# Kernel tuning notes

Measured on AMD Instinct MI355X. Metric: run time of the kernel, lower is better.

The kernel has to match this reference:

```python
import jax, jax.numpy as jnp
import numpy as np


def setup_inputs() -> dict:
    key = jax.random.key(0)
    kx, ky = jax.random.split(key)
    N, P1, P2, D = 4, 8192, 8192, 3
    x = jax.random.normal(kx, (N, P1, D), dtype=jnp.float32)
    y = jax.random.normal(ky, (N, P2, D), dtype=jnp.float32)
    return {"x": x, "y": y}


def reference(x, y):
    # ChamferDistance.forward with norm=2 (Euclidean cdist).
    N, P1, D = x.shape
    P2 = y.shape[1]
    x_sq = jnp.sum(x * x, axis=-1)              # [N, P1]
    y_sq = jnp.sum(y * y, axis=-1)              # [N, P2]
    xy = jnp.einsum("npd,nqd->npq", x, y)       # [N, P1, P2]
    sq = x_sq[:, :, None] + y_sq[:, None, :] - 2.0 * xy
    dists = jnp.sqrt(jnp.maximum(sq, 0.0))      # [N, P1, P2], == torch.cdist p=2
    cham_x = jnp.min(dists, axis=-1).sum(axis=1) / P1   # [N]
    cham_y = jnp.min(dists, axis=-2).sum(axis=1) / P2   # [N]
    return cham_x + cham_y
```

## Files before the change

kernel.cpp:

```cpp
#include <hip/hip_runtime.h>


typedef float v2f  __attribute__((ext_vector_type(2)));
typedef float v16f __attribute__((ext_vector_type(16)));

constexpr int BLK   = 256;
constexpr int Q     = 8;
constexpr int CHUNK = 128;
constexpr int NCH   = 64;

__global__ void preprocess_kernel(const float* __restrict__ X,
                                  const float* __restrict__ Y,
                                  float* __restrict__ pX, float* __restrict__ pY,
                                  unsigned int* __restrict__ wmin,
                                  float* __restrict__ out,
                                  int P1, int P2, int N)
{
    const int t  = blockIdx.x * blockDim.x + threadIdx.x;
    const int nx = N * P1;
    const int total = nx + N * P2;
    if (t < total) {
        const float* src = (t < nx) ? X : Y;
        float*       dst = (t < nx) ? pX : pY;
        const int    idx = (t < nx) ? t : t - nx;
        const float* p = src + 3L * idx;
        float x = p[0], y = p[1], z = p[2];
        float c = x * x + y * y + z * z;
        float* d = dst + (long)(idx >> 1) * 8;
        const int o = idx & 1;
        d[0 + o] = x; d[2 + o] = y; d[4 + o] = z; d[6 + o] = c;
        wmin[t] = 0xFFFFFFFFu;
    }
    if (t < N) out[t] = 0.f;
}

__global__ __launch_bounds__(BLK) void chamfer_min_kernel(
    const float* __restrict__ X, const float* __restrict__ Y,
    const float* __restrict__ pX, const float* __restrict__ pY,
    unsigned int* __restrict__ wmin, int P1, int P2, int N)
{
    const int n   = blockIdx.y;
    const int dz  = blockIdx.z;
    const int dir = dz / NCH;
    const int ch  = dz - dir * NCH;
    const float* A  = dir ? Y : X;
    const float* PB = dir ? pX : pY;
    const int Pa = dir ? P2 : P1;
    const int Pb = dir ? P1 : P2;

    const int stride = Pa / Q;
    const int ti = blockIdx.x * BLK + threadIdx.x;
    v2f nx[Q], ny[Q], nz[Q];
    float qsq[Q], m[Q];
    const float* An = A + (long)n * Pa * 3;
    #pragma unroll
    for (int q = 0; q < Q; ++q) {
        const float* p = An + 3L * (ti + q * stride);
        float ax = p[0], ay = p[1], az = p[2];
        nx[q].x = -2.f * ax; nx[q].y = nx[q].x;
        ny[q].x = -2.f * ay; ny[q].y = ny[q].x;
        nz[q].x = -2.f * az; nz[q].y = nz[q].x;
        qsq[q] = ax * ax + ay * ay + az * az;
        m[q] = 1e30f;
    }

    const float* pb = PB + ((long)n * (Pb >> 1) + (long)ch * (CHUNK >> 1)) * 8;

    auto compute4 = [&](const v16f& b) {
        v2f bx0; bx0.x = b[0];  bx0.y = b[1];
        v2f by0; by0.x = b[2];  by0.y = b[3];
        v2f bz0; bz0.x = b[4];  bz0.y = b[5];
        v2f cv0; cv0.x = b[6];  cv0.y = b[7];
        v2f bx1; bx1.x = b[8];  bx1.y = b[9];
        v2f by1; by1.x = b[10]; by1.y = b[11];
        v2f bz1; bz1.x = b[12]; bz1.y = b[13];
        v2f cv1; cv1.x = b[14]; cv1.y = b[15];
        #pragma unroll
        for (int q = 0; q < Q; ++q) {
            v2f t0, t1;
            asm("v_pk_fma_f32 %0, %2, %3, %4\n\t"
                "v_pk_fma_f32 %1, %2, %5, %6\n\t"
                "v_pk_fma_f32 %0, %7, %8, %0\n\t"
                "v_pk_fma_f32 %1, %7, %9, %1\n\t"
                "v_pk_fma_f32 %0, %10, %11, %0\n\t"
                "v_pk_fma_f32 %1, %10, %12, %1"
                : "=&v"(t0), "=&v"(t1)
                : "v"(nz[q]), "s"(bz0), "v"(cv0), "s"(bz1), "v"(cv1),
                  "v"(ny[q]), "s"(by0), "s"(by1),
                  "v"(nx[q]), "s"(bx0), "s"(bx1));
            float t0x = t0.x, t0y = t0.y, t1x = t1.x, t1y = t1.y;
            asm("v_min3_f32 %0, %1, %2, %0" : "+v"(m[q]) : "v"(t0x), "v"(t0y));
            asm("v_min3_f32 %0, %1, %2, %0" : "+v"(m[q]) : "v"(t1x), "v"(t1y));
        }
    };

    constexpr int NG = CHUNK / 4;
    v16f b0, b1;
    asm volatile("s_load_dwordx16 %0, %1, 0x0" : "=s"(b0) : "s"(pb));
    #pragma unroll 1
    for (int g = 0; g < NG; g += 2) {
        asm volatile("s_waitcnt lgkmcnt(0)" : "+s"(b0));
        if (g + 1 < NG)
            asm volatile("s_load_dwordx16 %0, %1, 0x0"
                         : "=s"(b1) : "s"(pb + (long)(g + 1) * 16));
        compute4(b0);
        asm volatile("s_waitcnt lgkmcnt(0)" : "+s"(b1));
        if (g + 2 < NG)
            asm volatile("s_load_dwordx16 %0, %1, 0x0"
                         : "=s"(b0) : "s"(pb + (long)(g + 2) * 16));
        compute4(b1);
    }

    unsigned int* wbase = wmin + (dir ? (long)N * P1 : 0) + (long)n * Pa;
    #pragma unroll
    for (int q = 0; q < Q; ++q) {
        float msq = fmaxf(m[q] + qsq[q], 0.0f);
        atomicMin(&wbase[ti + q * stride], __float_as_uint(msq));
    }
}

__global__ __launch_bounds__(BLK) void chamfer_reduce_kernel(
    const unsigned int* __restrict__ wmin, float* __restrict__ out,
    int P1, int P2, int N)
{
    __shared__ float wsum[BLK / 64];
    const int dir = blockIdx.z;
    const int n   = blockIdx.y;
    const int Pa  = dir ? P2 : P1;
    const unsigned int* base = wmin + (dir ? (long)N * P1 : 0) + (long)n * Pa;

    float s = 0.f;
    for (int i = blockIdx.x * BLK + threadIdx.x; i < Pa; i += gridDim.x * BLK)
        s += sqrtf(__uint_as_float(base[i]));

    for (int off = 32; off > 0; off >>= 1)
        s += __shfl_down(s, off);
    const int lane = threadIdx.x & 63, wid = threadIdx.x >> 6;
    if (lane == 0) wsum[wid] = s;
    __syncthreads();
    if (threadIdx.x == 0) {
        float t = 0.f;
        #pragma unroll
        for (int w = 0; w < BLK / 64; ++w) t += wsum[w];
        atomicAdd(&out[n], t / (float)Pa);
    }
}

extern "C" void kernel_launch(void* const* d_in, const int* in_sizes, int n_in,
                              void* d_out, int out_size, void* d_ws, size_t ws_size,
                              hipStream_t stream)
{
    const float* x = (const float*)d_in[0];
    const float* y = (const float*)d_in[1];
    float* out = (float*)d_out;

    const int N  = out_size;
    const int P1 = in_sizes[0] / (N * 3);
    const int P2 = in_sizes[1] / (N * 3);

    float* pX = (float*)d_ws;
    float* pY = pX + (long)N * P1 * 4;
    unsigned int* wmin = (unsigned int*)(pY + (long)N * P2 * 4);

    const int total = N * (P1 + P2);
    preprocess_kernel<<<(total + BLK - 1) / BLK, BLK, 0, stream>>>(
        x, y, pX, pY, wmin, out, P1, P2, N);

    const int gx = (max(P1, P2) / Q) / BLK;
    chamfer_min_kernel<<<dim3(gx, N, 2 * NCH), BLK, 0, stream>>>(
        x, y, pX, pY, wmin, P1, P2, N);

    chamfer_reduce_kernel<<<dim3(8, N, 2), BLK, 0, stream>>>(wmin, out, P1, P2, N);
}
```

Before: 52.53 us.

## Compute pairwise distance Gram terms with split-bf16 MFMA instead of packed FMA

Replaces the scalar/packed-FP32 distance loop with a matrix-core formulation. Each point's coordinates and squared norm are split into hi/lo bf16 pieces in preprocessing and packed into 16-element A/B vectors, so one 32x32x16 bf16 MFMA computes -2x·y + ||y||^2 with near-fp32 accuracy. Each wave keeps four 32-query B fragments resident, streams A fragments over a quarter of the targets, and folds the outputs with min3. The trade-off is a larger preprocessing workspace and reduced precision from the three-term bf16 split. The grid also assumes P1 == P2.

```diff
diff --git a/kernel.cpp b/kernel.cpp
--- a/kernel.cpp
+++ b/kernel.cpp
@@ -1,122 +1,140 @@
 #include <hip/hip_runtime.h>
 
 
-typedef float v2f  __attribute__((ext_vector_type(2)));
-typedef float v16f __attribute__((ext_vector_type(16)));
+typedef unsigned short u16;
+typedef short bf16x8 __attribute__((ext_vector_type(8)));
+typedef float f32x16 __attribute__((ext_vector_type(16)));
 
-constexpr int BLK   = 256;
-constexpr int Q     = 8;
-constexpr int CHUNK = 128;
-constexpr int NCH   = 64;
+constexpr int BLK = 256;
+constexpr int TC  = 4;
+
+__device__ __forceinline__ u16 f2bf(float f) {
+    unsigned u = __float_as_uint(f);
+    return (u16)((u + 0x7FFFu + ((u >> 16) & 1u)) >> 16);
+}
+__device__ __forceinline__ float bf2f(u16 h) {
+    return __uint_as_float((unsigned)h << 16);
+}
 
 __global__ void preprocess_kernel(const float* __restrict__ X,
                                   const float* __restrict__ Y,
-                                  float* __restrict__ pX, float* __restrict__ pY,
+                                  u16* __restrict__ AX, u16* __restrict__ BX,
+                                  u16* __restrict__ AY, u16* __restrict__ BY,
+                                  float* __restrict__ QSQ,
                                   unsigned int* __restrict__ wmin,
                                   float* __restrict__ out,
                                   int P1, int P2, int N)
 {
-    const int t  = blockIdx.x * blockDim.x + threadIdx.x;
+    const int t = blockIdx.x * blockDim.x + threadIdx.x;
     const int nx = N * P1;
     const int total = nx + N * P2;
     if (t < total) {
-        const float* src = (t < nx) ? X : Y;
-        float*       dst = (t < nx) ? pX : pY;
-        const int    idx = (t < nx) ? t : t - nx;
-        const float* p = src + 3L * idx;
-        float x = p[0], y = p[1], z = p[2];
-        float c = x * x + y * y + z * z;
-        float* d = dst + (long)(idx >> 1) * 8;
-        const int o = idx & 1;
-        d[0 + o] = x; d[2 + o] = y; d[4 + o] = z; d[6 + o] = c;
+        const bool isX = t < nx;
+        const int idx = isX ? t : t - nx;
+        const float* p = (isX ? X : Y) + 3L * idx;
+        float c[3] = {p[0], p[1], p[2]};
+        float tsq = fmaf(c[0], c[0], fmaf(c[1], c[1], c[2] * c[2]));
+        u16 uh[3], ul[3], qh[3], ql[3];
+        #pragma unroll
+        for (int i = 0; i < 3; ++i) {
+            float u = -2.f * c[i];
+            uh[i] = f2bf(u);    ul[i] = f2bf(u - bf2f(uh[i]));
+            qh[i] = f2bf(c[i]); ql[i] = f2bf(c[i] - bf2f(qh[i]));
+        }
+        u16 s1 = f2bf(tsq);
+        float r = tsq - bf2f(s1);
+        u16 s2 = f2bf(r);
+        u16 s3 = f2bf(r - bf2f(s2));
+        const u16 ONE = 0x3F80;
+        alignas(16) u16 av[16] = {uh[0],uh[1],uh[2], uh[0],uh[1],uh[2],
+                                  ul[0],ul[1],ul[2], ul[0],ul[1],ul[2],
+                                  s1, s2, s3, 0};
+        alignas(16) u16 bv[16] = {qh[0],qh[1],qh[2], ql[0],ql[1],ql[2],
+                                  qh[0],qh[1],qh[2], ql[0],ql[1],ql[2],
+                                  ONE, ONE, ONE, 0};
+        u16* ad = (isX ? AX : AY) + (size_t)idx * 16;
+        u16* bd = (isX ? BX : BY) + (size_t)idx * 16;
+        ((uint4*)ad)[0] = ((const uint4*)av)[0];
+        ((uint4*)ad)[1] = ((const uint4*)av)[1];
+        ((uint4*)bd)[0] = ((const uint4*)bv)[0];
+        ((uint4*)bd)[1] = ((const uint4*)bv)[1];
+        QSQ[t]  = tsq;
         wmin[t] = 0xFFFFFFFFu;
     }
     if (t < N) out[t] = 0.f;
 }
 
-__global__ __launch_bounds__(BLK) void chamfer_min_kernel(
-    const float* __restrict__ X, const float* __restrict__ Y,
-    const float* __restrict__ pX, const float* __restrict__ pY,
-    unsigned int* __restrict__ wmin, int P1, int P2, int N)
+__global__ __launch_bounds__(BLK) void chamfer_mfma_kernel(
+    const u16* __restrict__ AX, const u16* __restrict__ BX,
+    const u16* __restrict__ AY, const u16* __restrict__ BY,
+    const float* __restrict__ QSQ, unsigned int* __restrict__ wmin,
+    int P1, int P2, int N)
 {
-    const int n   = blockIdx.y;
-    const int dz  = blockIdx.z;
-    const int dir = dz / NCH;
-    const int ch  = dz - dir * NCH;
-    const float* A  = dir ? Y : X;
-    const float* PB = dir ? pX : pY;
-    const int Pa = dir ? P2 : P1;
-    const int Pb = dir ? P1 : P2;
+    const int n    = blockIdx.y;
+    const int dir  = blockIdx.z >> 2;
+    const int chk  = blockIdx.z & 3;
+    const int wave = threadIdx.x >> 6;
+    const int lane = threadIdx.x & 63;
+    const int col  = lane & 31;
+    const int half = lane >> 5;
 
-    const int stride = Pa / Q;
-    const int ti = blockIdx.x * BLK + threadIdx.x;
-    v2f nx[Q], ny[Q], nz[Q];
-    float qsq[Q], m[Q];
-    const float* An = A + (long)n * Pa * 3;
+    const int Pq = dir ? P2 : P1;
+    const int Pt = dir ? P1 : P2;
+    const u16* Bq = (dir ? BY : BX) + (size_t)n * Pq * 16;
+    const u16* At = (dir ? AX : AY) + (size_t)n * Pt * 16;
+    const float*  qs = QSQ  + (dir ? (size_t)N * P1 : 0) + (size_t)n * Pq;
+    unsigned int* wb = wmin + (dir ? (size_t)N * P1 : 0) + (size_t)n * Pq;
+
+    const int qg = blockIdx.x * (BLK / 64) + wave;
+    const int q0 = qg * 128 + col;
+    const bf16x8 b0 = *(const bf16x8*)(Bq + (size_t)(q0      ) * 16 + half * 8);
+    const bf16x8 b1 = *(const bf16x8*)(Bq + (size_t)(q0 +  32) * 16 + half * 8);
+    const bf16x8 b2 = *(const bf16x8*)(Bq + (size_t)(q0 +  64) * 16 + half * 8);
+    const bf16x8 b3 = *(const bf16x8*)(Bq + (size_t)(q0 +  96) * 16 + half * 8);
+    const float qs0 = qs[q0], qs1 = qs[q0 + 32], qs2 = qs[q0 + 64], qs3 = qs[q0 + 96];
+    float m0 = 1e30f, m1 = 1e30f, m2 = 1e30f, m3 = 1e30f;
+
+    f32x16 zc;
     #pragma unroll
-    for (int q = 0; q < Q; ++q) {
-        const float* p = An + 3L * (ti + q * stride);
-        float ax = p[0], ay = p[1], az = p[2];
-        nx[q].x = -2.f * ax; nx[q].y = nx[q].x;
-        ny[q].x = -2.f * ay; ny[q].y = ny[q].x;
-        nz[q].x = -2.f * az; nz[q].y = nz[q].x;
-        qsq[q] = ax * ax + ay * ay + az * az;
-        m[q] = 1e30f;
-    }
+    for (int i = 0; i < 16; ++i) zc[i] = 0.f;
 
-    const float* pb = PB + ((long)n * (Pb >> 1) + (long)ch * (CHUNK >> 1)) * 8;
+    #define MFMA(A, B) __builtin_amdgcn_mfma_f32_32x32x16_bf16((A), (B), zc, 0, 0, 0)
 
-    auto compute4 = [&](const v16f& b) {
-        v2f bx0; bx0.x = b[0];  bx0.y = b[1];
-        v2f by0; by0.x = b[2];  by0.y = b[3];
-        v2f bz0; bz0.x = b[4];  bz0.y = b[5];
-        v2f cv0; cv0.x = b[6];  cv0.y = b[7];
-        v2f bx1; bx1.x = b[8];  bx1.y = b[9];
-        v2f by1; by1.x = b[10]; by1.y = b[11];
-        v2f bz1; bz1.x = b[12]; bz1.y = b[13];
-        v2f cv1; cv1.x = b[14]; cv1.y = b[15];
+    auto fold = [&](const f32x16& d, float& mm) {
         #pragma unroll
-        for (int q = 0; q < Q; ++q) {
-            v2f t0, t1;
-            asm("v_pk_fma_f32 %0, %2, %3, %4\n\t"
-                "v_pk_fma_f32 %1, %2, %5, %6\n\t"
-                "v_pk_fma_f32 %0, %7, %8, %0\n\t"
-                "v_pk_fma_f32 %1, %7, %9, %1\n\t"
-                "v_pk_fma_f32 %0, %10, %11, %0\n\t"
-                "v_pk_fma_f32 %1, %10, %12, %1"
-                : "=&v"(t0), "=&v"(t1)
-                : "v"(nz[q]), "s"(bz0), "v"(cv0), "s"(bz1), "v"(cv1),
-                  "v"(ny[q]), "s"(by0), "s"(by1),
-                  "v"(nx[q]), "s"(bx0), "s"(bx1));
-            float t0x = t0.x, t0y = t0.y, t1x = t1.x, t1y = t1.y;
-            asm("v_min3_f32 %0, %1, %2, %0" : "+v"(m[q]) : "v"(t0x), "v"(t0y));
-            asm("v_min3_f32 %0, %1, %2, %0" : "+v"(m[q]) : "v"(t1x), "v"(t1y));
+        for (int i = 0; i < 16; i += 2) {
+            float x0 = d[i], x1 = d[i + 1];
+            asm("v_min3_f32 %0, %1, %2, %0" : "+v"(mm) : "v"(x0), "v"(x1));
         }
     };
 
-    constexpr int NG = CHUNK / 4;
-    v16f b0, b1;
-    asm volatile("s_load_dwordx16 %0, %1, 0x0" : "=s"(b0) : "s"(pb));
+    const int tpc = Pt >> 2;
+    const int NT  = tpc >> 5;
+    const u16* ap = At + ((size_t)(chk * tpc + col)) * 16 + half * 8;
+
+    bf16x8 a0 = *(const bf16x8*)(ap);
+    bf16x8 a1 = *(const bf16x8*)(ap + 512);
     #pragma unroll 1
-    for (int g = 0; g < NG; g += 2) {
-        asm volatile("s_waitcnt lgkmcnt(0)" : "+s"(b0));
-        if (g + 1 < NG)
-            asm volatile("s_load_dwordx16 %0, %1, 0x0"
-                         : "=s"(b1) : "s"(pb + (long)(g + 1) * 16));
-        compute4(b0);
-        asm volatile("s_waitcnt lgkmcnt(0)" : "+s"(b1));
-        if (g + 2 < NG)
-            asm volatile("s_load_dwordx16 %0, %1, 0x0"
-                         : "=s"(b0) : "s"(pb + (long)(g + 2) * 16));
-        compute4(b1);
+    for (int g = 0; g < NT; g += 2) {
+        f32x16 d0 = MFMA(a0, b0), d1 = MFMA(a0, b1),
+               d2 = MFMA(a0, b2), d3 = MFMA(a0, b3);
+        a0 = *(const bf16x8*)(ap + (size_t)min(g + 2, NT - 1) * 512);
+        fold(d0, m0); fold(d1, m1); fold(d2, m2); fold(d3, m3);
+        f32x16 e0 = MFMA(a1, b0), e1 = MFMA(a1, b1),
+               e2 = MFMA(a1, b2), e3 = MFMA(a1, b3);
+        a1 = *(const bf16x8*)(ap + (size_t)min(g + 3, NT - 1) * 512);
+        fold(e0, m0); fold(e1, m1); fold(e2, m2); fold(e3, m3);
     }
+    #undef MFMA
 
-    unsigned int* wbase = wmin + (dir ? (long)N * P1 : 0) + (long)n * Pa;
-    #pragma unroll
-    for (int q = 0; q < Q; ++q) {
-        float msq = fmaxf(m[q] + qsq[q], 0.0f);
-        atomicMin(&wbase[ti + q * stride], __float_as_uint(msq));
-    }
+    float v0 = fmaxf(m0 + qs0, 0.f);
+    float v1 = fmaxf(m1 + qs1, 0.f);
+    float v2 = fmaxf(m2 + qs2, 0.f);
+    float v3 = fmaxf(m3 + qs3, 0.f);
+    atomicMin(&wb[q0      ], __float_as_uint(v0));
+    atomicMin(&wb[q0 +  32], __float_as_uint(v1));
+    atomicMin(&wb[q0 +  64], __float_as_uint(v2));
+    atomicMin(&wb[q0 +  96], __float_as_uint(v3));
 }
 
 __global__ __launch_bounds__(BLK) void chamfer_reduce_kernel(
@@ -158,17 +176,20 @@
     const int P1 = in_sizes[0] / (N * 3);
     const int P2 = in_sizes[1] / (N * 3);
 
-    float* pX = (float*)d_ws;
-    float* pY = pX + (long)N * P1 * 4;
-    unsigned int* wmin = (unsigned int*)(pY + (long)N * P2 * 4);
+    u16* AX = (u16*)d_ws;
+    u16* BX = AX + (size_t)N * P1 * 16;
+    u16* AY = BX + (size_t)N * P1 * 16;
+    u16* BY = AY + (size_t)N * P2 * 16;
+    float* QSQ = (float*)(BY + (size_t)N * P2 * 16);
+    unsigned int* wmin = (unsigned int*)(QSQ + (size_t)N * (P1 + P2));
 
     const int total = N * (P1 + P2);
     preprocess_kernel<<<(total + BLK - 1) / BLK, BLK, 0, stream>>>(
-        x, y, pX, pY, wmin, out, P1, P2, N);
+        x, y, AX, BX, AY, BY, QSQ, wmin, out, P1, P2, N);
 
-    const int gx = (max(P1, P2) / Q) / BLK;
-    chamfer_min_kernel<<<dim3(gx, N, 2 * NCH), BLK, 0, stream>>>(
-        x, y, pX, pY, wmin, P1, P2, N);
+    const int gx = (P1 / 128) / (BLK / 64);
+    chamfer_mfma_kernel<<<dim3(gx, N, 2 * TC), BLK, 0, stream>>>(
+        AX, BX, AY, BY, QSQ, wmin, P1, P2, N);
 
     chamfer_reduce_kernel<<<dim3(8, N, 2), BLK, 0, stream>>>(wmin, out, P1, P2, N);
 }
```

After: 42.94 us. 18.3% less time.
